# Performance work log

Measured on AMD Instinct MI355X. Metric: run time of the kernel, lower is better.

Reference implementation:

```python
import jax, jax.numpy as jnp
import numpy as np

N = 100000
E = 1_600_000
IN_DIM = 128
HIDDEN = 128


def spmm(row, col, vals, H):
    # y[r] = sum_{edges e with row[e]==r} vals[e] * H[col[e]]
    msgs = vals[:, None] * H[col]          # [E, hidden] gather + scale
    return jax.ops.segment_sum(msgs, row, num_segments=H.shape[0])


def setup_inputs() -> dict:
    key = jax.random.key(0)
    ks = jax.random.split(key, 10)
    X = jax.random.normal(ks[0], (N, IN_DIM), dtype=jnp.float32)
    row = jax.random.randint(ks[1], (E,), 0, N, dtype=jnp.int32)
    col = jax.random.randint(ks[2], (E,), 0, N, dtype=jnp.int32)
    vals = jax.random.uniform(ks[3], (E,), dtype=jnp.float32)
    s_in = 1.0 / np.sqrt(IN_DIM)
    s_h = 1.0 / np.sqrt(HIDDEN)
    W_in = jax.random.normal(ks[4], (IN_DIM, HIDDEN), dtype=jnp.float32) * s_in
    b_in = jax.random.normal(ks[5], (HIDDEN,), dtype=jnp.float32) * s_in
    W_mp1 = jax.random.normal(ks[6], (HIDDEN, HIDDEN), dtype=jnp.float32) * s_h
    W_mp2 = jax.random.normal(ks[7], (HIDDEN, HIDDEN), dtype=jnp.float32) * s_h
    W_out = jax.random.normal(ks[8], (HIDDEN, 1), dtype=jnp.float32) * s_h
    b_out = jax.random.normal(ks[9], (1,), dtype=jnp.float32) * s_h
    return {"X": X, "row": row, "col": col, "vals": vals,
            "W_in": W_in, "b_in": b_in, "W_mp1": W_mp1, "W_mp2": W_mp2,
            "W_out": W_out, "b_out": b_out}


def reference(X, row, col, vals, W_in, b_in, W_mp1, W_mp2, W_out, b_out):
    H = jax.nn.relu(X @ W_in + b_in)          # [N, hidden]
    AH = spmm(row, col, vals, H)              # 1-hop propagation
    A2H = spmm(row, col, vals, AH)            # 2-hop propagation
    H2 = jax.nn.relu(AH @ W_mp1 + A2H @ W_mp2)
    return H2 @ W_out + b_out                 # [N, 1]
```

## Files before the change

### kernel.cpp

```cpp
#include <hip/hip_runtime.h>

#define N_NODES 100000
#define N_EDGES 1600000
#define NBUCK 391
#define NCHUNK 256
#define CHUNK 6250
#define LROW 136
#define DCAP 5120

typedef float f32x4 __attribute__((ext_vector_type(4)));
typedef _Float16 f16x8 __attribute__((ext_vector_type(8)));
typedef _Float16 h16x2 __attribute__((ext_vector_type(2)));

__device__ __forceinline__ unsigned f2h_bits(float f) {
    union { _Float16 h; unsigned short s; } c;
    c.h = (_Float16)f;
    return c.s;
}
__device__ __forceinline__ h16x2 u2h(unsigned u) {
    union { unsigned u; h16x2 h; } c;
    c.u = u;
    return c.h;
}
__device__ __forceinline__ unsigned pk16lo(unsigned hi, unsigned lo) {
    return __builtin_amdgcn_perm(hi, lo, 0x05040100u);
}
__device__ __forceinline__ unsigned pk16hi(unsigned hi, unsigned lo) {
    return __builtin_amdgcn_perm(hi, lo, 0x07060302u);
}
__device__ __forceinline__ float fdot2(h16x2 a, h16x2 b, float c) {
#if __has_builtin(__builtin_amdgcn_fdot2)
    return __builtin_amdgcn_fdot2(a, b, c, false);
#else
    return c + (float)a[0] * (float)b[0] + (float)a[1] * (float)b[1];
#endif
}

__device__ __forceinline__ f16x8 pack_h8(float4 a, float4 b) {
    f16x8 r;
    r[0] = (_Float16)a.x; r[1] = (_Float16)a.y;
    r[2] = (_Float16)a.z; r[3] = (_Float16)a.w;
    r[4] = (_Float16)b.x; r[5] = (_Float16)b.y;
    r[6] = (_Float16)b.z; r[7] = (_Float16)b.w;
    return r;
}


__global__ __launch_bounds__(256) void k_prep(const int* __restrict__ row,
                                              int* __restrict__ hmat,
                                              const float* __restrict__ Wa,
                                              const float* __restrict__ Wb,
                                              const float* __restrict__ Wc,
                                              unsigned short* __restrict__ Wta,
                                              unsigned short* __restrict__ Wtb,
                                              unsigned short* __restrict__ Wtc) {
    if (blockIdx.x < NCHUNK) {
        __shared__ int h[NBUCK];
        for (int i = threadIdx.x; i < NBUCK; i += 256) h[i] = 0;
        __syncthreads();
        int s = blockIdx.x * CHUNK, e = s + CHUNK;
        for (int i = s + threadIdx.x; i < e; i += 256)
            atomicAdd(&h[row[i] >> 8], 1);
        __syncthreads();
        for (int b = threadIdx.x; b < NBUCK; b += 256)
            hmat[blockIdx.x * NBUCK + b] = h[b];
    } else {
        int t = (blockIdx.x - NCHUNK) * 256 + threadIdx.x;
        int which = t >> 14;
        int i = t & 16383;
        int n = i & 127, k = i >> 7;
        const float* W = which == 0 ? Wa : which == 1 ? Wb : Wc;
        unsigned short* Wt = which == 0 ? Wta : which == 1 ? Wtb : Wtc;
        Wt[n * 128 + k] = (unsigned short)f2h_bits(W[k * 128 + n]);
    }
}

__global__ __launch_bounds__(512) void k_colscanB(const int* __restrict__ hmat,
                                                  int* __restrict__ bases,
                                                  int* __restrict__ bstart) {
    __shared__ int s[512];
    int b = blockIdx.x, t = threadIdx.x;
    if (b < NBUCK) {
        int v = (t < NCHUNK) ? hmat[t * NBUCK + b] : 0;
        s[t] = v;
        __syncthreads();
        for (int off = 1; off < 512; off <<= 1) {
            int x = (t >= off) ? s[t - off] : 0;
            __syncthreads();
            s[t] += x;
            __syncthreads();
        }
        if (t < NCHUNK) bases[t * NBUCK + b] = s[t] - v;
    } else {
        int v = 0;
        if (t < NBUCK) {
            for (int blk = 0; blk < NCHUNK; blk++) v += hmat[blk * NBUCK + t];
        }
        s[t] = v;
        __syncthreads();
        for (int off = 1; off < 512; off <<= 1) {
            int x = (t >= off) ? s[t - off] : 0;
            __syncthreads();
            s[t] += x;
            __syncthreads();
        }
        if (t < NBUCK) bstart[t] = s[t] - v;
        if (t == NBUCK) bstart[NBUCK] = N_EDGES;
    }
}

__global__ __launch_bounds__(256) void k_binC(const int* __restrict__ row,
                                              const int* __restrict__ col,
                                              const float* __restrict__ vals,
                                              const int* __restrict__ bstart,
                                              const int* __restrict__ bases,
                                              int2* __restrict__ grouped) {
    __shared__ int cnt[NBUCK];
    for (int i = threadIdx.x; i < NBUCK; i += 256) cnt[i] = 0;
    __syncthreads();
    int s = blockIdx.x * CHUNK, e = s + CHUNK;
    for (int i = s + threadIdx.x; i < e; i += 256) {
        int r = row[i];
        int b = r >> 8;
        int rank = atomicAdd(&cnt[b], 1);
        int pos = bstart[b] + bases[blockIdx.x * NBUCK + b] + rank;
        unsigned hv = f2h_bits(vals[i]);
        grouped[pos] = make_int2(col[i], ((r & 255) << 14) | hv);
    }
}

__global__ __launch_bounds__(256) void k_binD(const int2* __restrict__ grouped,
                                              const int* __restrict__ bstart,
                                              unsigned* __restrict__ evf,
                                              int* __restrict__ row_ptr) {
    __shared__ int h[256], sc[256], cur[256];
    __shared__ int2 ebuf[DCAP];
    int b = blockIdx.x, t = threadIdx.x;
    int s0 = bstart[b], e0 = bstart[b + 1];
    int n = e0 - s0;
    bool inlds = (n <= DCAP);
    h[t] = 0;
    __syncthreads();
    if (inlds) {
        for (int i = t; i < n; i += 256) ebuf[i] = grouped[s0 + i];
        __syncthreads();
        for (int i = t; i < n; i += 256)
            atomicAdd(&h[(ebuf[i].y >> 14) & 255], 1);
    } else {
        for (int i = s0 + t; i < e0; i += 256)
            atomicAdd(&h[(grouped[i].y >> 14) & 255], 1);
    }
    __syncthreads();
    int v = h[t];
    sc[t] = v;
    __syncthreads();
    for (int off = 1; off < 256; off <<= 1) {
        int x = (t >= off) ? sc[t - off] : 0;
        __syncthreads();
        sc[t] += x;
        __syncthreads();
    }
    int excl = sc[t] - v;
    cur[t] = excl;
    int grow = b * 256 + t;
    if (grow <= N_NODES) row_ptr[grow] = s0 + excl;
    __syncthreads();
    if (inlds) {
        for (int i = t; i < n; i += 256) {
            int2 g = ebuf[i];
            int rl = (g.y >> 14) & 255;
            int p = atomicAdd(&cur[rl], 1);
            evf[s0 + p] = ((unsigned)g.x << 14) | (unsigned)(g.y & 0x3fff);
        }
    } else {
        for (int i = s0 + t; i < e0; i += 256) {
            int2 g = grouped[i];
            int rl = (g.y >> 14) & 255;
            int p = atomicAdd(&cur[rl], 1);
            evf[s0 + p] = ((unsigned)g.x << 14) | (unsigned)(g.y & 0x3fff);
        }
    }
}

__global__ __launch_bounds__(256) void k_gemm_in(const float* __restrict__ X,
                                                 const unsigned short* __restrict__ Wt,
                                                 const float* __restrict__ b,
                                                 unsigned short* __restrict__ H) {
    __shared__ unsigned short lds[64 * LROW];
    int tid = threadIdx.x;
    int lane = tid & 63, wv = tid >> 6;
    int quad = lane >> 4, c16 = lane & 15;

    f16x8 wf[2][4];
    float bb[2];
#pragma unroll
    for (int nt = 0; nt < 2; nt++) {
        int ng = wv * 2 + nt;
        bb[nt] = b[ng * 16 + c16];
#pragma unroll
        for (int kc = 0; kc < 4; kc++)
            wf[nt][kc] = *(const f16x8*)&Wt[(ng * 16 + c16) * 128 + kc * 32 + quad * 8];
    }

    int tilebase = blockIdx.x * 64;
    const float4* Xg = (const float4*)X;
#pragma unroll
    for (int i = 0; i < 4; i++) {
        int c = tid + i * 256;
        int r = c >> 4, o = c & 15;
        int grow = tilebase + r;
        float4 f0 = make_float4(0.f, 0.f, 0.f, 0.f), f1 = f0;
        if (grow < N_NODES) {
            f0 = Xg[(size_t)grow * 32 + o * 2];
            f1 = Xg[(size_t)grow * 32 + o * 2 + 1];
        }
        *(f16x8*)&lds[r * LROW + o * 8] = pack_h8(f0, f1);
    }
    __syncthreads();

    f32x4 acc[4][2] = {};
#pragma unroll
    for (int t4 = 0; t4 < 4; t4++) {
#pragma unroll
        for (int kc = 0; kc < 4; kc++) {
            f16x8 af = *(const f16x8*)&lds[(t4 * 16 + c16) * LROW + kc * 32 + quad * 8];
#pragma unroll
            for (int nt = 0; nt < 2; nt++)
                acc[t4][nt] = __builtin_amdgcn_mfma_f32_16x16x32_f16(af, wf[nt][kc],
                                                                    acc[t4][nt], 0, 0, 0);
        }
    }
    __syncthreads();

#pragma unroll
    for (int t4 = 0; t4 < 4; t4++)
#pragma unroll
        for (int nt = 0; nt < 2; nt++) {
            int ncol = (wv * 2 + nt) * 16 + c16;
#pragma unroll
            for (int r = 0; r < 4; r++) {
                float v = fmaxf(acc[t4][nt][r] + bb[nt], 0.f);
                lds[(t4 * 16 + quad * 4 + r) * LROW + ncol] = (unsigned short)f2h_bits(v);
            }
        }
    __syncthreads();
#pragma unroll
    for (int i = 0; i < 4; i++) {
        int c = tid + i * 256;
        int r = c >> 4, o = c & 15;
        int grow = tilebase + r;
        if (grow < N_NODES)
            *(uint4*)&H[(size_t)grow * 128 + o * 8] = *(const uint4*)&lds[r * LROW + o * 8];
    }
}

__global__ __launch_bounds__(256) void k_spmm(const int* __restrict__ rp,
                                              const unsigned* __restrict__ evf,
                                              const unsigned* __restrict__ Hin,
                                              unsigned* __restrict__ Ho) {
    int wid = (blockIdx.x * blockDim.x + threadIdx.x) >> 6;
    int lane = threadIdx.x & 63;
    if (wid >= N_NODES) return;
    int q = lane >> 4, l16 = lane & 15;
    int s = __builtin_amdgcn_readfirstlane(rp[wid]);
    int e = __builtin_amdgcn_readfirstlane(rp[wid + 1]);
    float a0 = 0.f, a1 = 0.f, a2 = 0.f, a3 = 0.f;
    float a4 = 0.f, a5 = 0.f, a6 = 0.f, a7 = 0.f;
    for (int base = s; base < e; base += 64) {
        int cnt = e - base;
        if (cnt > 64) cnt = 64;
        unsigned ev = evf[base + (lane < cnt ? lane : cnt - 1)];
        int r = 0;
        for (; r + 16 <= cnt; r += 16) {
            unsigned u0 = __shfl(ev, r + q, 64);
            unsigned u1 = __shfl(ev, r + 4 + q, 64);
            unsigned u2 = __shfl(ev, r + 8 + q, 64);
            unsigned u3 = __shfl(ev, r + 12 + q, 64);
            const uint4 h0 = *(const uint4*)&Hin[(size_t)(u0 >> 14) * 64 + l16 * 4];
            const uint4 h1 = *(const uint4*)&Hin[(size_t)(u1 >> 14) * 64 + l16 * 4];
            const uint4 h2 = *(const uint4*)&Hin[(size_t)(u2 >> 14) * 64 + l16 * 4];
            const uint4 h3 = *(const uint4*)&Hin[(size_t)(u3 >> 14) * 64 + l16 * 4];
            h16x2 v01 = u2h(pk16lo(u1 & 0x3fffu, u0 & 0x3fffu));
            h16x2 v23 = u2h(pk16lo(u3 & 0x3fffu, u2 & 0x3fffu));
            a0 = fdot2(v01, u2h(pk16lo(h1.x, h0.x)), a0);
            a0 = fdot2(v23, u2h(pk16lo(h3.x, h2.x)), a0);
            a1 = fdot2(v01, u2h(pk16hi(h1.x, h0.x)), a1);
            a1 = fdot2(v23, u2h(pk16hi(h3.x, h2.x)), a1);
            a2 = fdot2(v01, u2h(pk16lo(h1.y, h0.y)), a2);
            a2 = fdot2(v23, u2h(pk16lo(h3.y, h2.y)), a2);
            a3 = fdot2(v01, u2h(pk16hi(h1.y, h0.y)), a3);
            a3 = fdot2(v23, u2h(pk16hi(h3.y, h2.y)), a3);
            a4 = fdot2(v01, u2h(pk16lo(h1.z, h0.z)), a4);
            a4 = fdot2(v23, u2h(pk16lo(h3.z, h2.z)), a4);
            a5 = fdot2(v01, u2h(pk16hi(h1.z, h0.z)), a5);
            a5 = fdot2(v23, u2h(pk16hi(h3.z, h2.z)), a5);
            a6 = fdot2(v01, u2h(pk16lo(h1.w, h0.w)), a6);
            a6 = fdot2(v23, u2h(pk16lo(h3.w, h2.w)), a6);
            a7 = fdot2(v01, u2h(pk16hi(h1.w, h0.w)), a7);
            a7 = fdot2(v23, u2h(pk16hi(h3.w, h2.w)), a7);
        }
        if (r < cnt) {
            int i0 = r + q, i1 = r + 4 + q, i2 = r + 8 + q, i3 = r + 12 + q;
            unsigned u0 = __shfl(ev, i0 < cnt ? i0 : cnt - 1, 64);
            unsigned u1 = __shfl(ev, i1 < cnt ? i1 : cnt - 1, 64);
            unsigned u2 = __shfl(ev, i2 < cnt ? i2 : cnt - 1, 64);
            unsigned u3 = __shfl(ev, i3 < cnt ? i3 : cnt - 1, 64);
            const uint4 h0 = *(const uint4*)&Hin[(size_t)(u0 >> 14) * 64 + l16 * 4];
            const uint4 h1 = *(const uint4*)&Hin[(size_t)(u1 >> 14) * 64 + l16 * 4];
            const uint4 h2 = *(const uint4*)&Hin[(size_t)(u2 >> 14) * 64 + l16 * 4];
            const uint4 h3 = *(const uint4*)&Hin[(size_t)(u3 >> 14) * 64 + l16 * 4];
            unsigned m0 = (i0 < cnt) ? (u0 & 0x3fffu) : 0u;
            unsigned m1 = (i1 < cnt) ? (u1 & 0x3fffu) : 0u;
            unsigned m2 = (i2 < cnt) ? (u2 & 0x3fffu) : 0u;
            unsigned m3 = (i3 < cnt) ? (u3 & 0x3fffu) : 0u;
            h16x2 v01 = u2h(pk16lo(m1, m0));
            h16x2 v23 = u2h(pk16lo(m3, m2));
            a0 = fdot2(v01, u2h(pk16lo(h1.x, h0.x)), a0);
            a0 = fdot2(v23, u2h(pk16lo(h3.x, h2.x)), a0);
            a1 = fdot2(v01, u2h(pk16hi(h1.x, h0.x)), a1);
            a1 = fdot2(v23, u2h(pk16hi(h3.x, h2.x)), a1);
            a2 = fdot2(v01, u2h(pk16lo(h1.y, h0.y)), a2);
            a2 = fdot2(v23, u2h(pk16lo(h3.y, h2.y)), a2);
            a3 = fdot2(v01, u2h(pk16hi(h1.y, h0.y)), a3);
            a3 = fdot2(v23, u2h(pk16hi(h3.y, h2.y)), a3);
            a4 = fdot2(v01, u2h(pk16lo(h1.z, h0.z)), a4);
            a4 = fdot2(v23, u2h(pk16lo(h3.z, h2.z)), a4);
            a5 = fdot2(v01, u2h(pk16hi(h1.z, h0.z)), a5);
            a5 = fdot2(v23, u2h(pk16hi(h3.z, h2.z)), a5);
            a6 = fdot2(v01, u2h(pk16lo(h1.w, h0.w)), a6);
            a6 = fdot2(v23, u2h(pk16lo(h3.w, h2.w)), a6);
            a7 = fdot2(v01, u2h(pk16hi(h1.w, h0.w)), a7);
            a7 = fdot2(v23, u2h(pk16hi(h3.w, h2.w)), a7);
        }
    }
    a0 += __shfl_xor(a0, 16, 64); a0 += __shfl_xor(a0, 32, 64);
    a1 += __shfl_xor(a1, 16, 64); a1 += __shfl_xor(a1, 32, 64);
    a2 += __shfl_xor(a2, 16, 64); a2 += __shfl_xor(a2, 32, 64);
    a3 += __shfl_xor(a3, 16, 64); a3 += __shfl_xor(a3, 32, 64);
    a4 += __shfl_xor(a4, 16, 64); a4 += __shfl_xor(a4, 32, 64);
    a5 += __shfl_xor(a5, 16, 64); a5 += __shfl_xor(a5, 32, 64);
    a6 += __shfl_xor(a6, 16, 64); a6 += __shfl_xor(a6, 32, 64);
    a7 += __shfl_xor(a7, 16, 64); a7 += __shfl_xor(a7, 32, 64);
    if (q == 0) {
        uint4 p;
        p.x = (f2h_bits(a1) << 16) | f2h_bits(a0);
        p.y = (f2h_bits(a3) << 16) | f2h_bits(a2);
        p.z = (f2h_bits(a5) << 16) | f2h_bits(a4);
        p.w = (f2h_bits(a7) << 16) | f2h_bits(a6);
        *(uint4*)&Ho[(size_t)wid * 64 + l16 * 4] = p;
    }
}

__global__ __launch_bounds__(256) void k_gemm_out(const unsigned short* __restrict__ AH,
                                                  const unsigned short* __restrict__ A2H,
                                                  const unsigned short* __restrict__ Wt1,
                                                  const unsigned short* __restrict__ Wt2,
                                                  const float* __restrict__ Wout,
                                                  const float* __restrict__ bout,
                                                  float* __restrict__ out) {
    __shared__ unsigned short lds[2][64 * LROW];
    __shared__ float part[4][64];
    int tid = threadIdx.x;
    int lane = tid & 63, wv = tid >> 6;
    int quad = lane >> 4, c16 = lane & 15;

    f16x8 w1f[2][4], w2f[2][4];
    float wo[2];
#pragma unroll
    for (int nt = 0; nt < 2; nt++) {
        int ng = wv * 2 + nt;
        wo[nt] = Wout[ng * 16 + c16];
#pragma unroll
        for (int kc = 0; kc < 4; kc++) {
            w1f[nt][kc] = *(const f16x8*)&Wt1[(ng * 16 + c16) * 128 + kc * 32 + quad * 8];
            w2f[nt][kc] = *(const f16x8*)&Wt2[(ng * 16 + c16) * 128 + kc * 32 + quad * 8];
        }
    }
    float bo = bout[0];

    int tilebase = blockIdx.x * 64;
    const uint4* Ag = (const uint4*)(AH + (size_t)tilebase * 128);
    const uint4* Bg = (const uint4*)(A2H + (size_t)tilebase * 128);
#pragma unroll
    for (int i = 0; i < 4; i++) {
        int c = tid + i * 256;
        int r = c >> 4, o = c & 15;
        *(uint4*)&lds[0][r * LROW + o * 8] = Ag[c];
        *(uint4*)&lds[1][r * LROW + o * 8] = Bg[c];
    }
    __syncthreads();

    f32x4 acc[4][2] = {};
#pragma unroll
    for (int t4 = 0; t4 < 4; t4++) {
#pragma unroll
        for (int kc = 0; kc < 4; kc++) {
            f16x8 afA = *(const f16x8*)&lds[0][(t4 * 16 + c16) * LROW + kc * 32 + quad * 8];
            f16x8 afB = *(const f16x8*)&lds[1][(t4 * 16 + c16) * LROW + kc * 32 + quad * 8];
#pragma unroll
            for (int nt = 0; nt < 2; nt++) {
                acc[t4][nt] = __builtin_amdgcn_mfma_f32_16x16x32_f16(afA, w1f[nt][kc],
                                                                    acc[t4][nt], 0, 0, 0);
                acc[t4][nt] = __builtin_amdgcn_mfma_f32_16x16x32_f16(afB, w2f[nt][kc],
                                                                    acc[t4][nt], 0, 0, 0);
            }
        }
    }

#pragma unroll
    for (int t4 = 0; t4 < 4; t4++) {
        float p[4];
#pragma unroll
        for (int r = 0; r < 4; r++)
            p[r] = fmaxf(acc[t4][0][r], 0.f) * wo[0] + fmaxf(acc[t4][1][r], 0.f) * wo[1];
#pragma unroll
        for (int m = 1; m < 16; m <<= 1)
#pragma unroll
            for (int r = 0; r < 4; r++) p[r] += __shfl_xor(p[r], m, 64);
        if (c16 == 0)
#pragma unroll
            for (int r = 0; r < 4; r++) part[wv][t4 * 16 + quad * 4 + r] = p[r];
    }
    __syncthreads();
    if (tid < 64) {
        int orow = tilebase + tid;
        if (orow < N_NODES)
            out[orow] = part[0][tid] + part[1][tid] + part[2][tid] + part[3][tid] + bo;
    }
}


extern "C" void kernel_launch(void* const* d_in, const int* in_sizes, int n_in,
                              void* d_out, int out_size, void* d_ws, size_t ws_size,
                              hipStream_t stream) {
    const float* X    = (const float*)d_in[0];
    const int*   row  = (const int*)d_in[1];
    const int*   col  = (const int*)d_in[2];
    const float* vals = (const float*)d_in[3];
    const float* W_in = (const float*)d_in[4];
    const float* b_in = (const float*)d_in[5];
    const float* W1   = (const float*)d_in[6];
    const float* W2   = (const float*)d_in[7];
    const float* Wout = (const float*)d_in[8];
    const float* bout = (const float*)d_in[9];
    float* out = (float*)d_out;

    char* ws = (char*)d_ws;
    size_t off = 0;
    auto alloc = [&](size_t bytes) -> void* {
        void* p = ws + off;
        off += (bytes + 511) & ~(size_t)511;
        return p;
    };
    unsigned short* Hb  = (unsigned short*)alloc((size_t)N_NODES * 128 * 2);
    unsigned short* AHb = (unsigned short*)alloc((size_t)N_NODES * 128 * 2);
    unsigned short* A2b = (unsigned short*)alloc((size_t)N_NODES * 128 * 2);
    unsigned* evf  = (unsigned*)alloc((size_t)N_EDGES * 4);
    int2* grouped  = (int2*)alloc((size_t)N_EDGES * 8);
    unsigned short* Wtin = (unsigned short*)alloc(128 * 128 * 2);
    unsigned short* Wt1  = (unsigned short*)alloc(128 * 128 * 2);
    unsigned short* Wt2  = (unsigned short*)alloc(128 * 128 * 2);
    int*   hmat    = (int*)alloc((size_t)NCHUNK * NBUCK * 4);
    int*   bases   = (int*)alloc((size_t)NCHUNK * NBUCK * 4);
    int*   bstart  = (int*)alloc(512 * 4);
    int*   row_ptr = (int*)alloc((size_t)(N_NODES + 256) * 4);

    k_prep<<<NCHUNK + 192, 256, 0, stream>>>(row, hmat, W_in, W1, W2, Wtin, Wt1, Wt2);
    k_colscanB<<<NBUCK + 1, 512, 0, stream>>>(hmat, bases, bstart);
    k_binC<<<NCHUNK, 256, 0, stream>>>(row, col, vals, bstart, bases, grouped);
    k_binD<<<NBUCK, 256, 0, stream>>>(grouped, bstart, evf, row_ptr);

    int gblk = (N_NODES + 63) / 64;
    k_gemm_in<<<gblk, 256, 0, stream>>>(X, Wtin, b_in, Hb);

    int sblk = (N_NODES + 3) / 4;
    k_spmm<<<sblk, 256, 0, stream>>>(row_ptr, evf, (const unsigned*)Hb, (unsigned*)AHb);
    k_spmm<<<sblk, 256, 0, stream>>>(row_ptr, evf, (const unsigned*)AHb, (unsigned*)A2b);

    k_gemm_out<<<gblk, 256, 0, stream>>>(AHb, A2b, Wt1, Wt2, Wout, bout, out);
}
```

Measured before the change: 305.2 us.

## Co-schedule input GEMM tiles with edge binning kernels via block-range split

Folds the input projection GEMM into the two binning kernels. Half of the GEMM tiles run as extra blocks alongside k_binC and the other half alongside k_binD, so the light, atomic-bound binning work overlaps with compute and one launch is removed. k_binC now caches its per-bucket base offsets in LDS instead of re-reading them from global memory for every edge. k_prep moves to 512-thread blocks. The cost is that the GEMM blocks now have the larger LDS footprint of the binning kernels, which may lower their occupancy.

```diff
diff --git a/kernel.cpp b/kernel.cpp
--- a/kernel.cpp
+++ b/kernel.cpp
@@ -7,6 +7,7 @@
 #define CHUNK 6250
 #define LROW 136
 #define DCAP 5120
+#define GSPLIT 782
 
 typedef float f32x4 __attribute__((ext_vector_type(4)));
 typedef _Float16 f16x8 __attribute__((ext_vector_type(8)));
@@ -45,8 +46,80 @@
     return r;
 }
 
-
-__global__ __launch_bounds__(256) void k_prep(const int* __restrict__ row,
+__device__ __forceinline__ void gemm_in_tile(int tilebase,
+                                             const float* __restrict__ X,
+                                             const unsigned short* __restrict__ Wt,
+                                             const float* __restrict__ bvec,
+                                             unsigned short* __restrict__ H,
+                                             unsigned short* lds) {
+    int tid = threadIdx.x;
+    int lane = tid & 63, wv = tid >> 6;
+    int quad = lane >> 4, c16 = lane & 15;
+
+    f16x8 wf[2][4];
+    float bb[2];
+#pragma unroll
+    for (int nt = 0; nt < 2; nt++) {
+        int ng = wv * 2 + nt;
+        bb[nt] = bvec[ng * 16 + c16];
+#pragma unroll
+        for (int kc = 0; kc < 4; kc++)
+            wf[nt][kc] = *(const f16x8*)&Wt[(ng * 16 + c16) * 128 + kc * 32 + quad * 8];
+    }
+
+    const float4* Xg = (const float4*)X;
+#pragma unroll
+    for (int i = 0; i < 4; i++) {
+        int c = tid + i * 256;
+        int r = c >> 4, o = c & 15;
+        int grow = tilebase + r;
+        float4 f0 = make_float4(0.f, 0.f, 0.f, 0.f), f1 = f0;
+        if (grow < N_NODES) {
+            f0 = Xg[(size_t)grow * 32 + o * 2];
+            f1 = Xg[(size_t)grow * 32 + o * 2 + 1];
+        }
+        *(f16x8*)&lds[r * LROW + o * 8] = pack_h8(f0, f1);
+    }
+    __syncthreads();
+
+    f32x4 acc[4][2] = {};
+#pragma unroll
+    for (int t4 = 0; t4 < 4; t4++) {
+#pragma unroll
+        for (int kc = 0; kc < 4; kc++) {
+            f16x8 af = *(const f16x8*)&lds[(t4 * 16 + c16) * LROW + kc * 32 + quad * 8];
+#pragma unroll
+            for (int nt = 0; nt < 2; nt++)
+                acc[t4][nt] = __builtin_amdgcn_mfma_f32_16x16x32_f16(af, wf[nt][kc],
+                                                                    acc[t4][nt], 0, 0, 0);
+        }
+    }
+    __syncthreads();
+
+#pragma unroll
+    for (int t4 = 0; t4 < 4; t4++)
+#pragma unroll
+        for (int nt = 0; nt < 2; nt++) {
+            int ncol = (wv * 2 + nt) * 16 + c16;
+#pragma unroll
+            for (int r = 0; r < 4; r++) {
+                float v = fmaxf(acc[t4][nt][r] + bb[nt], 0.f);
+                lds[(t4 * 16 + quad * 4 + r) * LROW + ncol] = (unsigned short)f2h_bits(v);
+            }
+        }
+    __syncthreads();
+#pragma unroll
+    for (int i = 0; i < 4; i++) {
+        int c = tid + i * 256;
+        int r = c >> 4, o = c & 15;
+        int grow = tilebase + r;
+        if (grow < N_NODES)
+            *(uint4*)&H[(size_t)grow * 128 + o * 8] = *(const uint4*)&lds[r * LROW + o * 8];
+    }
+}
+
+
+__global__ __launch_bounds__(512) void k_prep(const int* __restrict__ row,
                                               int* __restrict__ hmat,
                                               const float* __restrict__ Wa,
                                               const float* __restrict__ Wb,
@@ -56,16 +129,16 @@
                                               unsigned short* __restrict__ Wtc) {
     if (blockIdx.x < NCHUNK) {
         __shared__ int h[NBUCK];
-        for (int i = threadIdx.x; i < NBUCK; i += 256) h[i] = 0;
+        for (int i = threadIdx.x; i < NBUCK; i += 512) h[i] = 0;
         __syncthreads();
         int s = blockIdx.x * CHUNK, e = s + CHUNK;
-        for (int i = s + threadIdx.x; i < e; i += 256)
+        for (int i = s + threadIdx.x; i < e; i += 512)
             atomicAdd(&h[row[i] >> 8], 1);
         __syncthreads();
-        for (int b = threadIdx.x; b < NBUCK; b += 256)
+        for (int b = threadIdx.x; b < NBUCK; b += 512)
             hmat[blockIdx.x * NBUCK + b] = h[b];
     } else {
-        int t = (blockIdx.x - NCHUNK) * 256 + threadIdx.x;
+        int t = (blockIdx.x - NCHUNK) * 512 + threadIdx.x;
         int which = t >> 14;
         int i = t & 16383;
         int n = i & 127, k = i >> 7;
@@ -109,148 +182,102 @@
     }
 }
 
-__global__ __launch_bounds__(256) void k_binC(const int* __restrict__ row,
-                                              const int* __restrict__ col,
-                                              const float* __restrict__ vals,
-                                              const int* __restrict__ bstart,
-                                              const int* __restrict__ bases,
-                                              int2* __restrict__ grouped) {
-    __shared__ int cnt[NBUCK];
-    for (int i = threadIdx.x; i < NBUCK; i += 256) cnt[i] = 0;
-    __syncthreads();
-    int s = blockIdx.x * CHUNK, e = s + CHUNK;
-    for (int i = s + threadIdx.x; i < e; i += 256) {
-        int r = row[i];
-        int b = r >> 8;
-        int rank = atomicAdd(&cnt[b], 1);
-        int pos = bstart[b] + bases[blockIdx.x * NBUCK + b] + rank;
-        unsigned hv = f2h_bits(vals[i]);
-        grouped[pos] = make_int2(col[i], ((r & 255) << 14) | hv);
-    }
-}
-
-__global__ __launch_bounds__(256) void k_binD(const int2* __restrict__ grouped,
-                                              const int* __restrict__ bstart,
-                                              unsigned* __restrict__ evf,
-                                              int* __restrict__ row_ptr) {
-    __shared__ int h[256], sc[256], cur[256];
-    __shared__ int2 ebuf[DCAP];
-    int b = blockIdx.x, t = threadIdx.x;
-    int s0 = bstart[b], e0 = bstart[b + 1];
-    int n = e0 - s0;
-    bool inlds = (n <= DCAP);
-    h[t] = 0;
-    __syncthreads();
-    if (inlds) {
-        for (int i = t; i < n; i += 256) ebuf[i] = grouped[s0 + i];
-        __syncthreads();
-        for (int i = t; i < n; i += 256)
-            atomicAdd(&h[(ebuf[i].y >> 14) & 255], 1);
+__global__ __launch_bounds__(256) void k_binC_gemmA(const int* __restrict__ row,
+                                                    const int* __restrict__ col,
+                                                    const float* __restrict__ vals,
+                                                    const int* __restrict__ bstart,
+                                                    const int* __restrict__ bases,
+                                                    int2* __restrict__ grouped,
+                                                    const float* __restrict__ X,
+                                                    const unsigned short* __restrict__ Wt,
+                                                    const float* __restrict__ bvec,
+                                                    unsigned short* __restrict__ H) {
+    __shared__ __align__(16) char smraw[64 * LROW * 2];
+    if (blockIdx.x < NCHUNK) {
+        int* cnt = (int*)smraw;
+        int* basl = (int*)(smraw + 1600);
+        for (int i = threadIdx.x; i < NBUCK; i += 256) {
+            cnt[i] = 0;
+            basl[i] = bstart[i] + bases[blockIdx.x * NBUCK + i];
+        }
+        __syncthreads();
+        int s = blockIdx.x * CHUNK, e = s + CHUNK;
+        for (int i = s + threadIdx.x; i < e; i += 256) {
+            int r = row[i];
+            int b = r >> 8;
+            int rank = atomicAdd(&cnt[b], 1);
+            int pos = basl[b] + rank;
+            unsigned hv = f2h_bits(vals[i]);
+            grouped[pos] = make_int2(col[i], ((r & 255) << 14) | hv);
+        }
     } else {
-        for (int i = s0 + t; i < e0; i += 256)
-            atomicAdd(&h[(grouped[i].y >> 14) & 255], 1);
-    }
-    __syncthreads();
-    int v = h[t];
-    sc[t] = v;
-    __syncthreads();
-    for (int off = 1; off < 256; off <<= 1) {
-        int x = (t >= off) ? sc[t - off] : 0;
-        __syncthreads();
-        sc[t] += x;
-        __syncthreads();
-    }
-    int excl = sc[t] - v;
-    cur[t] = excl;
-    int grow = b * 256 + t;
-    if (grow <= N_NODES) row_ptr[grow] = s0 + excl;
-    __syncthreads();
-    if (inlds) {
-        for (int i = t; i < n; i += 256) {
-            int2 g = ebuf[i];
-            int rl = (g.y >> 14) & 255;
-            int p = atomicAdd(&cur[rl], 1);
-            evf[s0 + p] = ((unsigned)g.x << 14) | (unsigned)(g.y & 0x3fff);
+        gemm_in_tile((blockIdx.x - NCHUNK) * 64, X, Wt, bvec, H,
+                     (unsigned short*)smraw);
+    }
+}
+
+__global__ __launch_bounds__(256) void k_binD_gemmB(const int2* __restrict__ grouped,
+                                                    const int* __restrict__ bstart,
+                                                    unsigned* __restrict__ evf,
+                                                    int* __restrict__ row_ptr,
+                                                    const float* __restrict__ X,
+                                                    const unsigned short* __restrict__ Wt,
+                                                    const float* __restrict__ bvec,
+                                                    unsigned short* __restrict__ H) {
+    __shared__ __align__(16) char smraw[DCAP * 8 + 3 * 256 * 4];
+    if (blockIdx.x < NBUCK) {
+        int* h = (int*)smraw;
+        int* sc = h + 256;
+        int* cur = sc + 256;
+        int2* ebuf = (int2*)(smraw + 3 * 256 * 4);
+        int b = blockIdx.x, t = threadIdx.x;
+        int s0 = bstart[b], e0 = bstart[b + 1];
+        int n = e0 - s0;
+        bool inlds = (n <= DCAP);
+        h[t] = 0;
+        __syncthreads();
+        if (inlds) {
+            for (int i = t; i < n; i += 256) ebuf[i] = grouped[s0 + i];
+            __syncthreads();
+            for (int i = t; i < n; i += 256)
+                atomicAdd(&h[(ebuf[i].y >> 14) & 255], 1);
+        } else {
+            for (int i = s0 + t; i < e0; i += 256)
+                atomicAdd(&h[(grouped[i].y >> 14) & 255], 1);
+        }
+        __syncthreads();
+        int v = h[t];
+        sc[t] = v;
+        __syncthreads();
+        for (int off = 1; off < 256; off <<= 1) {
+            int x = (t >= off) ? sc[t - off] : 0;
+            __syncthreads();
+            sc[t] += x;
+            __syncthreads();
+        }
+        int excl = sc[t] - v;
+        cur[t] = excl;
+        int grow = b * 256 + t;
+        if (grow <= N_NODES) row_ptr[grow] = s0 + excl;
+        __syncthreads();
+        if (inlds) {
+            for (int i = t; i < n; i += 256) {
+                int2 g = ebuf[i];
+                int rl = (g.y >> 14) & 255;
+                int p = atomicAdd(&cur[rl], 1);
+                evf[s0 + p] = ((unsigned)g.x << 14) | (unsigned)(g.y & 0x3fff);
+            }
+        } else {
+            for (int i = s0 + t; i < e0; i += 256) {
+                int2 g = grouped[i];
+                int rl = (g.y >> 14) & 255;
+                int p = atomicAdd(&cur[rl], 1);
+                evf[s0 + p] = ((unsigned)g.x << 14) | (unsigned)(g.y & 0x3fff);
+            }
         }
     } else {
-        for (int i = s0 + t; i < e0; i += 256) {
-            int2 g = grouped[i];
-            int rl = (g.y >> 14) & 255;
-            int p = atomicAdd(&cur[rl], 1);
-            evf[s0 + p] = ((unsigned)g.x << 14) | (unsigned)(g.y & 0x3fff);
-        }
-    }
-}
-
-__global__ __launch_bounds__(256) void k_gemm_in(const float* __restrict__ X,
-                                                 const unsigned short* __restrict__ Wt,
-                                                 const float* __restrict__ b,
-                                                 unsigned short* __restrict__ H) {
-    __shared__ unsigned short lds[64 * LROW];
-    int tid = threadIdx.x;
-    int lane = tid & 63, wv = tid >> 6;
-    int quad = lane >> 4, c16 = lane & 15;
-
-    f16x8 wf[2][4];
-    float bb[2];
-#pragma unroll
-    for (int nt = 0; nt < 2; nt++) {
-        int ng = wv * 2 + nt;
-        bb[nt] = b[ng * 16 + c16];
-#pragma unroll
-        for (int kc = 0; kc < 4; kc++)
-            wf[nt][kc] = *(const f16x8*)&Wt[(ng * 16 + c16) * 128 + kc * 32 + quad * 8];
-    }
-
-    int tilebase = blockIdx.x * 64;
-    const float4* Xg = (const float4*)X;
-#pragma unroll
-    for (int i = 0; i < 4; i++) {
-        int c = tid + i * 256;
-        int r = c >> 4, o = c & 15;
-        int grow = tilebase + r;
-        float4 f0 = make_float4(0.f, 0.f, 0.f, 0.f), f1 = f0;
-        if (grow < N_NODES) {
-            f0 = Xg[(size_t)grow * 32 + o * 2];
-            f1 = Xg[(size_t)grow * 32 + o * 2 + 1];
-        }
-        *(f16x8*)&lds[r * LROW + o * 8] = pack_h8(f0, f1);
-    }
-    __syncthreads();
-
-    f32x4 acc[4][2] = {};
-#pragma unroll
-    for (int t4 = 0; t4 < 4; t4++) {
-#pragma unroll
-        for (int kc = 0; kc < 4; kc++) {
-            f16x8 af = *(const f16x8*)&lds[(t4 * 16 + c16) * LROW + kc * 32 + quad * 8];
-#pragma unroll
-            for (int nt = 0; nt < 2; nt++)
-                acc[t4][nt] = __builtin_amdgcn_mfma_f32_16x16x32_f16(af, wf[nt][kc],
-                                                                    acc[t4][nt], 0, 0, 0);
-        }
-    }
-    __syncthreads();
-
-#pragma unroll
-    for (int t4 = 0; t4 < 4; t4++)
-#pragma unroll
-        for (int nt = 0; nt < 2; nt++) {
-            int ncol = (wv * 2 + nt) * 16 + c16;
-#pragma unroll
-            for (int r = 0; r < 4; r++) {
-                float v = fmaxf(acc[t4][nt][r] + bb[nt], 0.f);
-                lds[(t4 * 16 + quad * 4 + r) * LROW + ncol] = (unsigned short)f2h_bits(v);
-            }
-        }
-    __syncthreads();
-#pragma unroll
-    for (int i = 0; i < 4; i++) {
-        int c = tid + i * 256;
-        int r = c >> 4, o = c & 15;
-        int grow = tilebase + r;
-        if (grow < N_NODES)
-            *(uint4*)&H[(size_t)grow * 128 + o * 8] = *(const uint4*)&lds[r * LROW + o * 8];
+        gemm_in_tile((GSPLIT + (int)blockIdx.x - NBUCK) * 64, X, Wt, bvec, H,
+                     (unsigned short*)smraw);
     }
 }
 
@@ -465,13 +492,14 @@
     int*   bstart  = (int*)alloc(512 * 4);
     int*   row_ptr = (int*)alloc((size_t)(N_NODES + 256) * 4);
 
-    k_prep<<<NCHUNK + 192, 256, 0, stream>>>(row, hmat, W_in, W1, W2, Wtin, Wt1, Wt2);
+    int gblk = (N_NODES + 63) / 64;
+
+    k_prep<<<NCHUNK + 96, 512, 0, stream>>>(row, hmat, W_in, W1, W2, Wtin, Wt1, Wt2);
     k_colscanB<<<NBUCK + 1, 512, 0, stream>>>(hmat, bases, bstart);
-    k_binC<<<NCHUNK, 256, 0, stream>>>(row, col, vals, bstart, bases, grouped);
-    k_binD<<<NBUCK, 256, 0, stream>>>(grouped, bstart, evf, row_ptr);
-
-    int gblk = (N_NODES + 63) / 64;
-    k_gemm_in<<<gblk, 256, 0, stream>>>(X, Wtin, b_in, Hb);
+    k_binC_gemmA<<<NCHUNK + GSPLIT, 256, 0, stream>>>(row, col, vals, bstart, bases,
+                                                      grouped, X, Wtin, b_in, Hb);
+    k_binD_gemmB<<<NBUCK + (gblk - GSPLIT), 256, 0, stream>>>(grouped, bstart, evf,
+                                                              row_ptr, X, Wtin, b_in, Hb);
 
     int sblk = (N_NODES + 3) / 4;
     k_spmm<<<sblk, 256, 0, stream>>>(row_ptr, evf, (const unsigned*)Hb, (unsigned*)AHb);
```

New measurement: 301.8 us. Within noise of the previous version (-1.1%).
